# Kernel tuning notes

Hardware: AMD Instinct MI355X
Metric: run time of the kernel (lower is better)

The kernel has to match this reference:

```python
import jax, jax.numpy as jnp
import numpy as np

T = 8          # message-passing steps (hparams['T'])
D = 64         # link_state_dim
R = 128        # readout_units
E = 100000     # num edges (rows of link_state)
M = 400000     # num messages (len of states_first/second)
G = 1000       # num graphs in the batch


def _gru_cell(x, h, W, U, b):
    """Keras GRUCell with reset_after=True. x:[N,in], h:[N,units].
    W:[in,3u], U:[u,3u], b:[2,3u] (input bias, recurrent bias)."""
    mx = x @ W + b[0]
    mh = h @ U + b[1]
    xz, xr, xh = jnp.split(mx, 3, axis=-1)
    hz, hr, hh = jnp.split(mh, 3, axis=-1)
    z = jax.nn.sigmoid(xz + hz)
    r = jax.nn.sigmoid(xr + hr)
    cand = jnp.tanh(xh + r * hh)
    return z * h + (1.0 - z) * cand


def setup_inputs() -> dict:
    key = jax.random.key(0)
    ks = jax.random.split(key, 12)
    glorot = jax.nn.initializers.glorot_uniform()
    inp = {
        "link_state": jax.random.normal(ks[0], (E, D), jnp.float32),
        "states_first": jax.random.randint(ks[1], (M,), 0, E, jnp.int32),
        "states_second": jax.random.randint(ks[2], (M,), 0, E, jnp.int32),
        "states_graph_ids": jnp.sort(jax.random.randint(ks[3], (E,), 0, G, jnp.int32)),
        "num_edges": E,
        # Message MLP: Dense(D) with selu on concat [*, 2D]
        "W_msg": glorot(ks[4], (2 * D, D), jnp.float32),
        "b_msg": jnp.zeros((D,), jnp.float32),
        # Update GRUCell (units=D, input dim=D)
        "W_upd": glorot(ks[5], (D, 3 * D), jnp.float32),
        "U_upd": glorot(ks[6], (D, 3 * D), jnp.float32),
        "b_upd": jnp.zeros((2, 3 * D), jnp.float32),
        # Readout GRU (units=R, input dim=D)
        "W_ro": glorot(ks[7], (D, 3 * R), jnp.float32),
        "U_ro": glorot(ks[8], (R, 3 * R), jnp.float32),
        "b_ro": jnp.zeros((2, 3 * R), jnp.float32),
        # Final Dense(1)
        "W_out": glorot(ks[9], (R, 1), jnp.float32),
        "b_out": jnp.zeros((1,), jnp.float32),
    }
    return inp


def reference(link_state, states_first, states_second, states_graph_ids, num_edges,
              W_msg, b_msg, W_upd, U_upd, b_upd, W_ro, U_ro, b_ro, W_out, b_out):
    def mp_step(h, _):
        # gather sender/receiver states, concat -> message MLP (selu)
        edges_concat = jnp.concatenate([h[states_first], h[states_second]], axis=1)  # [M, 2D]
        msg = jax.nn.selu(edges_concat @ W_msg + b_msg)                              # [M, D]
        # scatter-add messages to receiver edges
        agg = jax.ops.segment_sum(msg, states_second, num_segments=num_edges)        # [E, D]
        h_new = _gru_cell(agg, h, W_upd, U_upd, b_upd)                               # [E, D]
        return h_new, h_new

    _, seq = jax.lax.scan(mp_step, link_state, None, length=T)  # seq: [T, E, D]

    # Readout GRU over the T-step state sequence per edge; return last hidden state
    def ro_step(h, x_t):
        h_new = _gru_cell(x_t, h, W_ro, U_ro, b_ro)
        return h_new, None

    h0 = jnp.zeros((link_state.shape[0], R), link_state.dtype)
    historial, _ = jax.lax.scan(ro_step, h0, seq)               # [E, R]

    # sorted segment_sum over graph ids, then Dense(1)
    per_graph = jax.ops.segment_sum(historial, states_graph_ids, num_segments=G,
                                    indices_are_sorted=True)    # [G, R]
    return per_graph @ W_out + b_out                             # [G, 1]
```

## Files before the change

### kernel.cpp

```cpp
#include <hip/hip_runtime.h>
#include <hip/hip_bf16.h>

#define D 64
#define R 128
#define NSTEPS 8
#define SELU_SCALE 1.0507009873554805f
#define SELU_ALPHA 1.6732632423543772f
#define PADH 72
#define PADF 68
#define PADR 136

typedef _Float16 half8 __attribute__((ext_vector_type(8)));
typedef float f32x4 __attribute__((ext_vector_type(4)));

__device__ __forceinline__ float fast_sig(float x) {
    return __fdividef(1.0f, 1.0f + __expf(-x));
}
__device__ __forceinline__ float fast_tanh(float x) {
    float xc = fminf(fmaxf(x, -15.0f), 15.0f);
    float e = __expf(2.0f * xc);
    return 1.0f - __fdividef(2.0f, e + 1.0f);
}

__global__ __launch_bounds__(256) void swizzle_all(
    const float* __restrict__ Wm, const float* __restrict__ Wu,
    const float* __restrict__ Uu, const float* __restrict__ Wr,
    const float* __restrict__ Ur,
    _Float16* __restrict__ wWm, _Float16* __restrict__ wWu,
    _Float16* __restrict__ wUu, _Float16* __restrict__ wWr,
    _Float16* __restrict__ wUr)
{
    const float* src; _Float16* dst; int K, N;
    switch (blockIdx.y) {
        case 0: src = Wm; dst = wWm; K = 128; N = 64;  break;
        case 1: src = Wu; dst = wWu; K = 64;  N = 192; break;
        case 2: src = Uu; dst = wUu; K = 64;  N = 192; break;
        case 3: src = Wr; dst = wWr; K = 64;  N = 384; break;
        default: src = Ur; dst = wUr; K = 128; N = 384; break;
    }
    int idx = blockIdx.x * 256 + threadIdx.x;
    int KT = K >> 5;
    int total = KT * (N >> 4) * 512;
    if (idx >= total) return;
    int j = idx & 7;
    int lane = (idx >> 3) & 63;
    int kt = (idx >> 9) % KT;
    int nt = idx / (512 * KT);
    int k = 32 * kt + 8 * (lane >> 4) + j;
    int n = 16 * nt + (lane & 15);
    dst[idx] = (_Float16)src[(size_t)k * N + n];
}

__global__ __launch_bounds__(256) void h16_init(const float* __restrict__ src,
                                                _Float16* __restrict__ dst, int n) {
    int i = blockIdx.x * 256 + threadIdx.x;
    if (i < n) dst[i] = (_Float16)src[i];
}

__global__ __launch_bounds__(192) void bias_pack(const float* __restrict__ bu,
                                                 const float* __restrict__ brr,
                                                 float4* __restrict__ biasU,
                                                 float4* __restrict__ biasR) {
    int c = threadIdx.x;
    if (c < 64) {
        biasU[c] = make_float4(bu[c] + bu[192 + c], bu[64 + c] + bu[256 + c],
                               bu[128 + c], bu[320 + c]);
    } else {
        int cr = c - 64;
        biasR[cr] = make_float4(brr[cr] + brr[384 + cr], brr[128 + cr] + brr[512 + cr],
                                brr[256 + cr], brr[640 + cr]);
    }
}

__global__ __launch_bounds__(256) void hist_kernel(const int* __restrict__ second,
                                                   int* __restrict__ cnt, int M) {
    int m = blockIdx.x * 256 + threadIdx.x;
    if (m < M) atomicAdd(&cnt[second[m]], 1);
}

__global__ __launch_bounds__(256) void scan_bsum(const int* __restrict__ cnt,
                                                 int* __restrict__ bsum, int E) {
    int i = blockIdx.x * 256 + threadIdx.x;
    int tid = threadIdx.x;
    int v = (i < E) ? cnt[i] : 0;
    __shared__ int s[256];
    s[tid] = v;
    __syncthreads();
    #pragma unroll
    for (int d = 1; d < 256; d <<= 1) {
        int t = (tid >= d) ? s[tid - d] : 0;
        __syncthreads();
        s[tid] += t;
        __syncthreads();
    }
    if (tid == 255) bsum[blockIdx.x] = s[255];
}

__global__ __launch_bounds__(1024) void scan_part(int* __restrict__ bsum, int NB) {
    int tid = threadIdx.x;
    __shared__ int s[1024];
    int v = (tid < NB) ? bsum[tid] : 0;
    s[tid] = v;
    __syncthreads();
    #pragma unroll
    for (int d = 1; d < 1024; d <<= 1) {
        int t = (tid >= d) ? s[tid - d] : 0;
        __syncthreads();
        s[tid] += t;
        __syncthreads();
    }
    if (tid < NB) bsum[tid] = s[tid] - v;
}

__global__ __launch_bounds__(256) void scan_final(const int* __restrict__ cnt,
                                                  const int* __restrict__ bsum,
                                                  int* __restrict__ off, int E) {
    int i = blockIdx.x * 256 + threadIdx.x;
    int tid = threadIdx.x;
    int v = (i < E) ? cnt[i] : 0;
    __shared__ int s[256];
    s[tid] = v;
    __syncthreads();
    #pragma unroll
    for (int d = 1; d < 256; d <<= 1) {
        int t = (tid >= d) ? s[tid - d] : 0;
        __syncthreads();
        s[tid] += t;
        __syncthreads();
    }
    if (i < E) off[i] = bsum[blockIdx.x] + s[tid] - v;
}

__global__ __launch_bounds__(256) void scatter_kernel(const int* __restrict__ second,
                                                      const int* __restrict__ off,
                                                      int* __restrict__ cur,
                                                      int* __restrict__ perm, int M) {
    int m = blockIdx.x * 256 + threadIdx.x;
    if (m < M) {
        int s = second[m];
        int p = atomicAdd(&cur[s], 1);
        perm[off[s] + p] = m;
    }
}

__global__ __launch_bounds__(256) void bucket_sort(const int* __restrict__ off,
                                                   int* __restrict__ perm,
                                                   int E, int M) {
    int e = blockIdx.x * 256 + threadIdx.x;
    if (e >= E) return;
    int a = off[e];
    int b = (e == E - 1) ? M : off[e + 1];
    for (int i = a + 1; i < b; ++i) {
        int key = perm[i];
        int j = i - 1;
        while (j >= a && perm[j] > key) {
            perm[j + 1] = perm[j];
            --j;
        }
        perm[j + 1] = key;
    }
}

__global__ __launch_bounds__(256) void fs_pack(const int* __restrict__ first,
                                               const int* __restrict__ second,
                                               const int* __restrict__ perm,
                                               int2* __restrict__ fs, int M) {
    int m = blockIdx.x * 256 + threadIdx.x;
    if (m < M) {
        int pm = perm[m];
        fs[m] = make_int2(first[pm], second[pm]);
    }
}

__global__ __launch_bounds__(256) void msg_upd(
    const _Float16* __restrict__ hin,
    _Float16* __restrict__ hout,
    const int2* __restrict__ fs,
    const int* __restrict__ off,
    const half8* __restrict__ wBm,
    const float* __restrict__ bm,
    const half8* __restrict__ wWu,
    const half8* __restrict__ wUu,
    const float4* __restrict__ biasU,
    int E, int M)
{
    __shared__ _Float16 stage_s[4][16 * PADH];
    __shared__ float aggF_s[4][16 * PADF];
    __shared__ int skeys[4][16];

    const int wid = threadIdx.x >> 6;
    const int lane = threadIdx.x & 63;
    const int hi = lane >> 4;
    const int l15 = lane & 15;
    const int e0 = (blockIdx.x * 4 + wid) * 16;

    _Float16* stageH = stage_s[wid];
    float* aggF = aggF_s[wid];
    int* skey = skeys[wid];

    #pragma unroll
    for (int m = 0; m < 16; ++m)
        aggF[m * PADF + lane] = 0.0f;

    half8 Bm[4][4];
    #pragma unroll
    for (int nt = 0; nt < 4; ++nt)
        #pragma unroll
        for (int kt = 0; kt < 4; ++kt)
            Bm[nt][kt] = wBm[(nt * 4 + kt) * 64 + lane];

    if (e0 >= E) return;

    {
        int b = min(e0 + 16, E);
        int mstart = off[e0];
        int mend = (b == E) ? M : off[b];

        #pragma unroll 1
        for (int ch = 0; mstart + ch * 16 < mend; ++ch) {
            int mrow = mstart + ch * 16 + l15;
            bool mv = (mrow < mend);
            int mcl = min(mrow, mend - 1);
            int2 p = fs[mcl];
            const half8* fr = reinterpret_cast<const half8*>(hin + (size_t)p.x * D);
            const half8* sr = reinterpret_cast<const half8*>(hin + (size_t)p.y * D);
            half8 A[4];
            A[0] = fr[hi];
            A[1] = fr[4 + hi];
            A[2] = sr[hi];
            A[3] = sr[4 + hi];

            f32x4 acc[4];
            #pragma unroll
            for (int nt = 0; nt < 4; ++nt) acc[nt] = (f32x4){0.f, 0.f, 0.f, 0.f};
            #pragma unroll
            for (int nt = 0; nt < 4; ++nt)
                #pragma unroll
                for (int kt = 0; kt < 4; ++kt)
                    acc[nt] = __builtin_amdgcn_mfma_f32_16x16x32_f16(A[kt], Bm[nt][kt], acc[nt], 0, 0, 0);

            #pragma unroll
            for (int nt = 0; nt < 4; ++nt) {
                int n = nt * 16 + l15;
                float bias = bm[n];
                #pragma unroll
                for (int r = 0; r < 4; ++r) {
                    float v = acc[nt][r] + bias;
                    v = (v > 0.0f) ? (SELU_SCALE * v)
                                   : (SELU_SCALE * SELU_ALPHA) * (__expf(v) - 1.0f);
                    stageH[(hi * 4 + r) * PADH + n] = (_Float16)v;
                }
            }
            if (lane < 16) skey[lane] = mv ? (p.y - e0) : -1;

            float run = 0.0f;
            int kprev = skey[0];
            #pragma unroll
            for (int m = 0; m < 16; ++m) {
                int km = skey[m];
                if (km != kprev) {
                    if (kprev >= 0) aggF[kprev * PADF + lane] += run;
                    run = 0.0f;
                    kprev = km;
                }
                run += (float)stageH[m * PADH + lane];
            }
            if (kprev >= 0) aggF[kprev * PADF + lane] += run;
        }
    }

    const int ec = min(e0 + l15, E - 1);

    half8 AX[2], AHu[2];
    #pragma unroll
    for (int kt = 0; kt < 2; ++kt) {
        const float* s = aggF + l15 * PADF + 32 * kt + 8 * hi;
        half8 ax;
        #pragma unroll
        for (int j = 0; j < 8; ++j) ax[j] = (_Float16)s[j];
        AX[kt] = ax;
        AHu[kt] = reinterpret_cast<const half8*>(hin + (size_t)ec * D)[4 * kt + hi];
    }

    #pragma unroll 1
    for (int i = 0; i < 4; ++i) {
        half8 WBz[2], WBr[2], WBc[2], UBz[2], UBr[2], UBc[2];
        #pragma unroll
        for (int kt = 0; kt < 2; ++kt) {
            WBz[kt] = wWu[((0 + i) * 2 + kt) * 64 + lane];
            WBr[kt] = wWu[((4 + i) * 2 + kt) * 64 + lane];
            WBc[kt] = wWu[((8 + i) * 2 + kt) * 64 + lane];
            UBz[kt] = wUu[((0 + i) * 2 + kt) * 64 + lane];
            UBr[kt] = wUu[((4 + i) * 2 + kt) * 64 + lane];
            UBc[kt] = wUu[((8 + i) * 2 + kt) * 64 + lane];
        }
        int n = 16 * i + l15;
        float4 bU = biasU[n];

        f32x4 az  = (f32x4){0.f, 0.f, 0.f, 0.f};
        f32x4 ar_ = (f32x4){0.f, 0.f, 0.f, 0.f};
        f32x4 acx = (f32x4){0.f, 0.f, 0.f, 0.f};
        f32x4 ach = (f32x4){0.f, 0.f, 0.f, 0.f};
        #pragma unroll
        for (int kt = 0; kt < 2; ++kt) {
            az  = __builtin_amdgcn_mfma_f32_16x16x32_f16(AX[kt], WBz[kt], az, 0, 0, 0);
            az  = __builtin_amdgcn_mfma_f32_16x16x32_f16(AHu[kt], UBz[kt], az, 0, 0, 0);
            ar_ = __builtin_amdgcn_mfma_f32_16x16x32_f16(AX[kt], WBr[kt], ar_, 0, 0, 0);
            ar_ = __builtin_amdgcn_mfma_f32_16x16x32_f16(AHu[kt], UBr[kt], ar_, 0, 0, 0);
            acx = __builtin_amdgcn_mfma_f32_16x16x32_f16(AX[kt], WBc[kt], acx, 0, 0, 0);
            ach = __builtin_amdgcn_mfma_f32_16x16x32_f16(AHu[kt], UBc[kt], ach, 0, 0, 0);
        }
        #pragma unroll
        for (int r = 0; r < 4; ++r) {
            int e = e0 + hi * 4 + r;
            int ecl = min(e, E - 1);
            float z = fast_sig(az[r] + bU.x);
            float rr = fast_sig(ar_[r] + bU.y);
            float c = fast_tanh(acx[r] + bU.z + rr * (ach[r] + bU.w));
            float hp = (float)hin[(size_t)ecl * D + n];
            float hn = z * hp + (1.0f - z) * c;
            if (e < E) hout[(size_t)e * D + n] = (_Float16)hn;
        }
    }
}

__global__ __launch_bounds__(256) void ro_all(
    const _Float16* __restrict__ hseq1,
    const int* __restrict__ gid,
    const float* __restrict__ Wout,
    const half8* __restrict__ wWr,
    const half8* __restrict__ wUr,
    const float4* __restrict__ biasR,
    float* __restrict__ out,
    int E, int edelems)
{
    __shared__ _Float16 rotile_s[4][16 * PADR];

    const int wid = threadIdx.x >> 6;
    const int lane = threadIdx.x & 63;
    const int hi = lane >> 4;
    const int l15 = lane & 15;
    const int e0 = (blockIdx.x * 4 + wid) * 16;
    if (e0 >= E) return;

    _Float16* rotile = rotile_s[wid];
    const int ec = min(e0 + l15, E - 1);

    half8 hpC0 = {}, hpC1 = {}, hpC2 = {}, hpC3 = {};

    #pragma unroll 1
    for (int t = 0; t < NSTEPS; ++t) {
        const _Float16* ht = hseq1 + (size_t)t * edelems;

        half8 AXt[2];
        #pragma unroll
        for (int kt = 0; kt < 2; ++kt)
            AXt[kt] = reinterpret_cast<const half8*>(ht + (size_t)ec * D)[4 * kt + hi];

        #pragma unroll
        for (int q = 0; q < 4; ++q) {
            half8 cur;
            switch (q) {
                case 0: cur = hpC0; break;
                case 1: cur = hpC1; break;
                case 2: cur = hpC2; break;
                default: cur = hpC3; break;
            }
            #pragma unroll
            for (int jj = 0; jj < 8; ++jj) {
                int it = 2 * q + (jj >> 2);
                int r = jj & 3;
                rotile[(hi * 4 + r) * PADR + it * 16 + l15] = cur[jj];
            }
        }
        half8 AHro[4];
        #pragma unroll
        for (int kt = 0; kt < 4; ++kt)
            AHro[kt] = *reinterpret_cast<const half8*>(&rotile[l15 * PADR + 32 * kt + 8 * hi]);

        #pragma unroll 1
        for (int q = 0; q < 4; ++q) {
            half8 cur;
            switch (q) {
                case 0: cur = hpC0; break;
                case 1: cur = hpC1; break;
                case 2: cur = hpC2; break;
                default: cur = hpC3; break;
            }
            half8 nxt;
            #pragma unroll
            for (int par = 0; par < 2; ++par) {
                int it = 2 * q + par;
                half8 WBz[2], WBr[2], WBx[2], UBz[4], UBr[4], UBh[4];
                #pragma unroll
                for (int kt = 0; kt < 2; ++kt) {
                    WBz[kt] = wWr[((0 + it) * 2 + kt) * 64 + lane];
                    WBr[kt] = wWr[((8 + it) * 2 + kt) * 64 + lane];
                    WBx[kt] = wWr[((16 + it) * 2 + kt) * 64 + lane];
                }
                #pragma unroll
                for (int kt = 0; kt < 4; ++kt) {
                    UBz[kt] = wUr[((0 + it) * 4 + kt) * 64 + lane];
                    UBr[kt] = wUr[((8 + it) * 4 + kt) * 64 + lane];
                    UBh[kt] = wUr[((16 + it) * 4 + kt) * 64 + lane];
                }
                int c = it * 16 + l15;
                float4 bR = biasR[c];

                f32x4 az  = (f32x4){0.f, 0.f, 0.f, 0.f};
                f32x4 ar_ = (f32x4){0.f, 0.f, 0.f, 0.f};
                f32x4 acx = (f32x4){0.f, 0.f, 0.f, 0.f};
                f32x4 ach = (f32x4){0.f, 0.f, 0.f, 0.f};
                #pragma unroll
                for (int kt = 0; kt < 2; ++kt) {
                    az  = __builtin_amdgcn_mfma_f32_16x16x32_f16(AXt[kt], WBz[kt], az, 0, 0, 0);
                    ar_ = __builtin_amdgcn_mfma_f32_16x16x32_f16(AXt[kt], WBr[kt], ar_, 0, 0, 0);
                    acx = __builtin_amdgcn_mfma_f32_16x16x32_f16(AXt[kt], WBx[kt], acx, 0, 0, 0);
                }
                #pragma unroll
                for (int kt = 0; kt < 4; ++kt) {
                    az  = __builtin_amdgcn_mfma_f32_16x16x32_f16(AHro[kt], UBz[kt], az, 0, 0, 0);
                    ar_ = __builtin_amdgcn_mfma_f32_16x16x32_f16(AHro[kt], UBr[kt], ar_, 0, 0, 0);
                    ach = __builtin_amdgcn_mfma_f32_16x16x32_f16(AHro[kt], UBh[kt], ach, 0, 0, 0);
                }
                #pragma unroll
                for (int r = 0; r < 4; ++r) {
                    float z = fast_sig(az[r] + bR.x);
                    float rr = fast_sig(ar_[r] + bR.y);
                    float cc = fast_tanh(acx[r] + bR.z + rr * (ach[r] + bR.w));
                    float hp = (float)cur[par * 4 + r];
                    float hn = z * hp + (1.0f - z) * cc;
                    nxt[par * 4 + r] = (_Float16)hn;
                }
            }
            switch (q) {
                case 0: hpC0 = nxt; break;
                case 1: hpC1 = nxt; break;
                case 2: hpC2 = nxt; break;
                default: hpC3 = nxt; break;
            }
        }
    }

    float wv[8];
    #pragma unroll
    for (int it = 0; it < 8; ++it) wv[it] = Wout[it * 16 + l15];

    float part[4] = {0.f, 0.f, 0.f, 0.f};
    #pragma unroll
    for (int q = 0; q < 4; ++q) {
        half8 cur;
        switch (q) {
            case 0: cur = hpC0; break;
            case 1: cur = hpC1; break;
            case 2: cur = hpC2; break;
            default: cur = hpC3; break;
        }
        #pragma unroll
        for (int jj = 0; jj < 8; ++jj) {
            int it = 2 * q + (jj >> 2);
            int r = jj & 3;
            part[r] = fmaf((float)cur[jj], wv[it], part[r]);
        }
    }
    #pragma unroll
    for (int d = 1; d < 16; d <<= 1) {
        #pragma unroll
        for (int r = 0; r < 4; ++r)
            part[r] += __shfl_xor(part[r], d);
    }
    if (l15 == 0) {
        #pragma unroll
        for (int r = 0; r < 4; ++r) {
            int e = e0 + hi * 4 + r;
            if (e < E) unsafeAtomicAdd(out + gid[e], part[r]);
        }
    }
}

__global__ void out_init_kernel(float* __restrict__ out, const float* __restrict__ b_out, int G) {
    int g = blockIdx.x * blockDim.x + threadIdx.x;
    if (g < G) out[g] = b_out[0];
}

extern "C" void kernel_launch(void* const* d_in, const int* in_sizes, int n_in,
                              void* d_out, int out_size, void* d_ws, size_t ws_size,
                              hipStream_t stream) {
    const float* link_state = (const float*)d_in[0];
    const int*   first      = (const int*)d_in[1];
    const int*   second     = (const int*)d_in[2];
    const int*   gids       = (const int*)d_in[3];
    const float* Wm         = (const float*)d_in[5];
    const float* bm         = (const float*)d_in[6];
    const float* Wu         = (const float*)d_in[7];
    const float* Uu         = (const float*)d_in[8];
    const float* bu         = (const float*)d_in[9];
    const float* Wr         = (const float*)d_in[10];
    const float* Ur         = (const float*)d_in[11];
    const float* brb        = (const float*)d_in[12];
    const float* Wout       = (const float*)d_in[13];
    const float* bout       = (const float*)d_in[14];

    const int E = in_sizes[0] / D;
    const int M = in_sizes[1];
    const int G = out_size;

    char* p = (char*)d_ws;
    auto carve = [&](size_t bytes) {
        void* r = (void*)p;
        p += (bytes + 255) & ~(size_t)255;
        return r;
    };
    const size_t edelems = (size_t)E * D;
    _Float16*  hseq  = (_Float16*)carve(edelems * 2 * (NSTEPS + 1));
    int*       perm  = (int*)carve((size_t)M * 4);
    int2*      fs    = (int2*)carve((size_t)M * 8);
    int*       cnt   = (int*)carve((size_t)E * 4);
    int*       cur   = (int*)carve((size_t)E * 4);
    int*       off   = (int*)carve((size_t)(E + 1) * 4);
    int*       bsum  = (int*)carve(4096 * 4);
    _Float16*  wWm   = (_Float16*)carve(8192 * 2);
    _Float16*  wWu   = (_Float16*)carve(12288 * 2);
    _Float16*  wUu   = (_Float16*)carve(12288 * 2);
    _Float16*  wWr   = (_Float16*)carve(24576 * 2);
    _Float16*  wUr   = (_Float16*)carve(49152 * 2);
    float4*    biasU = (float4*)carve(64 * 16);
    float4*    biasR = (float4*)carve(128 * 16);

    hipMemsetAsync(cnt, 0, (size_t)E * 4, stream);
    hipMemsetAsync(cur, 0, (size_t)E * 4, stream);

    h16_init<<<(E * D + 255) / 256, 256, 0, stream>>>(link_state, hseq, E * D);
    swizzle_all<<<dim3(192, 5), 256, 0, stream>>>(Wm, Wu, Uu, Wr, Ur,
                                                  wWm, wWu, wUu, wWr, wUr);
    bias_pack<<<1, 192, 0, stream>>>(bu, brb, biasU, biasR);

    const int NB = (E + 255) / 256;
    hist_kernel<<<(M + 255) / 256, 256, 0, stream>>>(second, cnt, M);
    scan_bsum<<<NB, 256, 0, stream>>>(cnt, bsum, E);
    scan_part<<<1, 1024, 0, stream>>>(bsum, NB);
    scan_final<<<NB, 256, 0, stream>>>(cnt, bsum, off, E);
    scatter_kernel<<<(M + 255) / 256, 256, 0, stream>>>(second, off, cur, perm, M);
    bucket_sort<<<NB, 256, 0, stream>>>(off, perm, E, M);
    fs_pack<<<(M + 255) / 256, 256, 0, stream>>>(first, second, perm, fs, M);

    const int e_blocks = (E + 63) / 64;

    for (int t = 0; t < NSTEPS; ++t) {
        msg_upd<<<e_blocks, 256, 0, stream>>>(hseq + (size_t)t * edelems,
                                              hseq + (size_t)(t + 1) * edelems,
                                              fs, off,
                                              (const half8*)wWm, bm,
                                              (const half8*)wWu, (const half8*)wUu, biasU,
                                              E, M);
    }

    out_init_kernel<<<(G + 255) / 256, 256, 0, stream>>>((float*)d_out, bout, G);
    ro_all<<<e_blocks, 256, 0, stream>>>(hseq + edelems, gids, Wout,
                                         (const half8*)wWr, (const half8*)wUr, biasR,
                                         (float*)d_out, E, (int)edelems);
}
```

Measured before the change: 876.3 us.

## Split readout GRU output columns across 8 waves per 16-edge block

The readout GRU kernel now gives each block one 16-edge tile and has 8 waves each own 16 of the 128 output units, instead of one wave looping over all 128 units. Each wave keeps its slice of the W/U weights in registers for all 8 steps rather than reloading them every step. The hidden state is exchanged through a shared LDS tile with two barriers per step, and the per-edge output dot product is reduced across waves in LDS before the atomic add. This adds block-wide synchronisation and repeats the input-state loads in every wave.

```diff
diff --git a/kernel.cpp b/kernel.cpp
--- a/kernel.cpp
+++ b/kernel.cpp
@@ -324,7 +324,7 @@
     }
 }
 
-__global__ __launch_bounds__(256) void ro_all(
+__global__ __launch_bounds__(512, 2) void ro_all(
     const _Float16* __restrict__ hseq1,
     const int* __restrict__ gid,
     const float* __restrict__ Wout,
@@ -334,135 +334,83 @@
     float* __restrict__ out,
     int E, int edelems)
 {
-    __shared__ _Float16 rotile_s[4][16 * PADR];
-
-    const int wid = threadIdx.x >> 6;
+    __shared__ _Float16 rotile[16 * PADR];
+    __shared__ float partials[8][16];
+
+    const int w = threadIdx.x >> 6;
     const int lane = threadIdx.x & 63;
     const int hi = lane >> 4;
     const int l15 = lane & 15;
-    const int e0 = (blockIdx.x * 4 + wid) * 16;
-    if (e0 >= E) return;
-
-    _Float16* rotile = rotile_s[wid];
+    const int e0 = blockIdx.x * 16;
     const int ec = min(e0 + l15, E - 1);
 
-    half8 hpC0 = {}, hpC1 = {}, hpC2 = {}, hpC3 = {};
+    half8 WBz[2], WBr[2], WBx[2], UBz[4], UBr[4], UBh[4];
+    #pragma unroll
+    for (int kt = 0; kt < 2; ++kt) {
+        WBz[kt] = wWr[((0 + w) * 2 + kt) * 64 + lane];
+        WBr[kt] = wWr[((8 + w) * 2 + kt) * 64 + lane];
+        WBx[kt] = wWr[((16 + w) * 2 + kt) * 64 + lane];
+    }
+    #pragma unroll
+    for (int kt = 0; kt < 4; ++kt) {
+        UBz[kt] = wUr[((0 + w) * 4 + kt) * 64 + lane];
+        UBr[kt] = wUr[((8 + w) * 4 + kt) * 64 + lane];
+        UBh[kt] = wUr[((16 + w) * 4 + kt) * 64 + lane];
+    }
+    const int c = w * 16 + l15;
+    const float4 bR = biasR[c];
+
+    half8 hp = {};
 
     #pragma unroll 1
     for (int t = 0; t < NSTEPS; ++t) {
+        #pragma unroll
+        for (int r = 0; r < 4; ++r)
+            rotile[(hi * 4 + r) * PADR + w * 16 + l15] = hp[r];
+        __syncthreads();
+
+        half8 AHro[4];
+        #pragma unroll
+        for (int kt = 0; kt < 4; ++kt)
+            AHro[kt] = *reinterpret_cast<const half8*>(&rotile[l15 * PADR + 32 * kt + 8 * hi]);
+        __syncthreads();
+
         const _Float16* ht = hseq1 + (size_t)t * edelems;
-
         half8 AXt[2];
         #pragma unroll
         for (int kt = 0; kt < 2; ++kt)
             AXt[kt] = reinterpret_cast<const half8*>(ht + (size_t)ec * D)[4 * kt + hi];
 
-        #pragma unroll
-        for (int q = 0; q < 4; ++q) {
-            half8 cur;
-            switch (q) {
-                case 0: cur = hpC0; break;
-                case 1: cur = hpC1; break;
-                case 2: cur = hpC2; break;
-                default: cur = hpC3; break;
-            }
-            #pragma unroll
-            for (int jj = 0; jj < 8; ++jj) {
-                int it = 2 * q + (jj >> 2);
-                int r = jj & 3;
-                rotile[(hi * 4 + r) * PADR + it * 16 + l15] = cur[jj];
-            }
-        }
-        half8 AHro[4];
-        #pragma unroll
-        for (int kt = 0; kt < 4; ++kt)
-            AHro[kt] = *reinterpret_cast<const half8*>(&rotile[l15 * PADR + 32 * kt + 8 * hi]);
-
-        #pragma unroll 1
-        for (int q = 0; q < 4; ++q) {
-            half8 cur;
-            switch (q) {
-                case 0: cur = hpC0; break;
-                case 1: cur = hpC1; break;
-                case 2: cur = hpC2; break;
-                default: cur = hpC3; break;
-            }
-            half8 nxt;
-            #pragma unroll
-            for (int par = 0; par < 2; ++par) {
-                int it = 2 * q + par;
-                half8 WBz[2], WBr[2], WBx[2], UBz[4], UBr[4], UBh[4];
-                #pragma unroll
-                for (int kt = 0; kt < 2; ++kt) {
-                    WBz[kt] = wWr[((0 + it) * 2 + kt) * 64 + lane];
-                    WBr[kt] = wWr[((8 + it) * 2 + kt) * 64 + lane];
-                    WBx[kt] = wWr[((16 + it) * 2 + kt) * 64 + lane];
-                }
-                #pragma unroll
-                for (int kt = 0; kt < 4; ++kt) {
-                    UBz[kt] = wUr[((0 + it) * 4 + kt) * 64 + lane];
-                    UBr[kt] = wUr[((8 + it) * 4 + kt) * 64 + lane];
-                    UBh[kt] = wUr[((16 + it) * 4 + kt) * 64 + lane];
-                }
-                int c = it * 16 + l15;
-                float4 bR = biasR[c];
-
-                f32x4 az  = (f32x4){0.f, 0.f, 0.f, 0.f};
-                f32x4 ar_ = (f32x4){0.f, 0.f, 0.f, 0.f};
-                f32x4 acx = (f32x4){0.f, 0.f, 0.f, 0.f};
-                f32x4 ach = (f32x4){0.f, 0.f, 0.f, 0.f};
-                #pragma unroll
-                for (int kt = 0; kt < 2; ++kt) {
-                    az  = __builtin_amdgcn_mfma_f32_16x16x32_f16(AXt[kt], WBz[kt], az, 0, 0, 0);
-                    ar_ = __builtin_amdgcn_mfma_f32_16x16x32_f16(AXt[kt], WBr[kt], ar_, 0, 0, 0);
-                    acx = __builtin_amdgcn_mfma_f32_16x16x32_f16(AXt[kt], WBx[kt], acx, 0, 0, 0);
-                }
-                #pragma unroll
-                for (int kt = 0; kt < 4; ++kt) {
-                    az  = __builtin_amdgcn_mfma_f32_16x16x32_f16(AHro[kt], UBz[kt], az, 0, 0, 0);
-                    ar_ = __builtin_amdgcn_mfma_f32_16x16x32_f16(AHro[kt], UBr[kt], ar_, 0, 0, 0);
-                    ach = __builtin_amdgcn_mfma_f32_16x16x32_f16(AHro[kt], UBh[kt], ach, 0, 0, 0);
-                }
-                #pragma unroll
-                for (int r = 0; r < 4; ++r) {
-                    float z = fast_sig(az[r] + bR.x);
-                    float rr = fast_sig(ar_[r] + bR.y);
-                    float cc = fast_tanh(acx[r] + bR.z + rr * (ach[r] + bR.w));
-                    float hp = (float)cur[par * 4 + r];
-                    float hn = z * hp + (1.0f - z) * cc;
-                    nxt[par * 4 + r] = (_Float16)hn;
-                }
-            }
-            switch (q) {
-                case 0: hpC0 = nxt; break;
-                case 1: hpC1 = nxt; break;
-                case 2: hpC2 = nxt; break;
-                default: hpC3 = nxt; break;
-            }
-        }
-    }
-
-    float wv[8];
-    #pragma unroll
-    for (int it = 0; it < 8; ++it) wv[it] = Wout[it * 16 + l15];
-
-    float part[4] = {0.f, 0.f, 0.f, 0.f};
-    #pragma unroll
-    for (int q = 0; q < 4; ++q) {
-        half8 cur;
-        switch (q) {
-            case 0: cur = hpC0; break;
-            case 1: cur = hpC1; break;
-            case 2: cur = hpC2; break;
-            default: cur = hpC3; break;
-        }
-        #pragma unroll
-        for (int jj = 0; jj < 8; ++jj) {
-            int it = 2 * q + (jj >> 2);
-            int r = jj & 3;
-            part[r] = fmaf((float)cur[jj], wv[it], part[r]);
-        }
-    }
+        f32x4 az  = (f32x4){0.f, 0.f, 0.f, 0.f};
+        f32x4 ar_ = (f32x4){0.f, 0.f, 0.f, 0.f};
+        f32x4 acx = (f32x4){0.f, 0.f, 0.f, 0.f};
+        f32x4 ach = (f32x4){0.f, 0.f, 0.f, 0.f};
+        #pragma unroll
+        for (int kt = 0; kt < 2; ++kt) {
+            az  = __builtin_amdgcn_mfma_f32_16x16x32_f16(AXt[kt], WBz[kt], az, 0, 0, 0);
+            ar_ = __builtin_amdgcn_mfma_f32_16x16x32_f16(AXt[kt], WBr[kt], ar_, 0, 0, 0);
+            acx = __builtin_amdgcn_mfma_f32_16x16x32_f16(AXt[kt], WBx[kt], acx, 0, 0, 0);
+        }
+        #pragma unroll
+        for (int kt = 0; kt < 4; ++kt) {
+            az  = __builtin_amdgcn_mfma_f32_16x16x32_f16(AHro[kt], UBz[kt], az, 0, 0, 0);
+            ar_ = __builtin_amdgcn_mfma_f32_16x16x32_f16(AHro[kt], UBr[kt], ar_, 0, 0, 0);
+            ach = __builtin_amdgcn_mfma_f32_16x16x32_f16(AHro[kt], UBh[kt], ach, 0, 0, 0);
+        }
+        #pragma unroll
+        for (int r = 0; r < 4; ++r) {
+            float z = fast_sig(az[r] + bR.x);
+            float rr = fast_sig(ar_[r] + bR.y);
+            float cc = fast_tanh(acx[r] + bR.z + rr * (ach[r] + bR.w));
+            float hpf = (float)hp[r];
+            hp[r] = (_Float16)(z * hpf + (1.0f - z) * cc);
+        }
+    }
+
+    const float wv = Wout[c];
+    float part[4];
+    #pragma unroll
+    for (int r = 0; r < 4; ++r) part[r] = (float)hp[r] * wv;
     #pragma unroll
     for (int d = 1; d < 16; d <<= 1) {
         #pragma unroll
@@ -471,10 +419,16 @@
     }
     if (l15 == 0) {
         #pragma unroll
-        for (int r = 0; r < 4; ++r) {
-            int e = e0 + hi * 4 + r;
-            if (e < E) unsafeAtomicAdd(out + gid[e], part[r]);
-        }
+        for (int r = 0; r < 4; ++r)
+            partials[w][hi * 4 + r] = part[r];
+    }
+    __syncthreads();
+    if (w == 0 && lane < 16) {
+        float s = 0.0f;
+        #pragma unroll
+        for (int ww = 0; ww < 8; ++ww) s += partials[ww][lane];
+        int e = e0 + lane;
+        if (e < E) unsafeAtomicAdd(out + gid[e], s);
     }
 }
 
@@ -556,7 +510,8 @@
     }
 
     out_init_kernel<<<(G + 255) / 256, 256, 0, stream>>>((float*)d_out, bout, G);
-    ro_all<<<e_blocks, 256, 0, stream>>>(hseq + edelems, gids, Wout,
-                                         (const half8*)wWr, (const half8*)wUr, biasR,
-                                         (float*)d_out, E, (int)edelems);
-}
+    const int ro_blocks = (E + 15) / 16;
+    ro_all<<<ro_blocks, 512, 0, stream>>>(hseq + edelems, gids, Wout,
+                                          (const half8*)wWr, (const half8*)wUr, biasR,
+                                          (float*)d_out, E, (int)edelems);
+}
```

Measured after the change: 806.0 us. -8.0%, faster.
